# Performance work log

Hardware: AMD Instinct MI355X
Metric: run time of the kernel (lower is better)

The kernel has to match this reference:

```python
import jax, jax.numpy as jnp
import numpy as np

N = 50000      # nodes
E = 1000000    # edges (avg degree 20)
IN, H, OUT = 3, 128, 3


def setup_inputs() -> dict:
    key = jax.random.key(0)
    ks = jax.random.split(key, 12)
    pos = jax.random.normal(ks[0], (N, IN), dtype=jnp.float32)
    edge_index = jax.random.randint(ks[1], (2, E), 0, N, dtype=jnp.int64)
    dims = [(IN, H), (H, H), (H, H), (H, H), (H, OUT)]
    inp = {"pos": pos, "edge_index": edge_index}
    for i, (di, do) in enumerate(dims):
        inp[f"W{i}"] = jax.random.normal(ks[2 + 2 * i], (di, do), dtype=jnp.float32) / np.sqrt(di).astype(np.float32)
        inp[f"b{i}"] = jnp.zeros((do,), dtype=jnp.float32)
    return inp


def _gcn_conv(x, W, b, src, dst, norm):
    # PyG GCNConv: linear transform first, then normalized scatter-add, then bias
    h = x @ W                                  # [N, do]
    msg = h[src] * norm[:, None]               # gather + edge-normalize  [E+N, do]
    out = jax.ops.segment_sum(msg, dst, num_segments=N)  # scatter-add to targets
    return out + b


def reference(pos, edge_index, W0, b0, W1, b1, W2, b2, W3, b3, W4, b4):
    src, dst = edge_index[0], edge_index[1]
    loop = jnp.arange(N, dtype=src.dtype)
    src = jnp.concatenate([src, loop])         # add self-loops
    dst = jnp.concatenate([dst, loop])
    # symmetric normalization: deg computed on target nodes incl. self-loops
    deg = jax.ops.segment_sum(jnp.ones_like(src, dtype=pos.dtype), dst, num_segments=N)
    dis = jnp.where(deg > 0, jax.lax.rsqrt(jnp.maximum(deg, 1e-12)), 0.0)
    norm = dis[src] * dis[dst]                 # [E+N]

    Ws = [W0, W1, W2, W3, W4]
    bs = [b0, b1, b2, b3, b4]
    x = pos
    for i in range(4):                         # all but last layer: conv + SiLU
        x = jax.nn.silu(_gcn_conv(x, Ws[i], bs[i], src, dst, norm))
    return _gcn_conv(x, Ws[4], bs[4], src, dst, norm)
```

## Files before the change

kernel.cpp:

```cpp
#include <hip/hip_runtime.h>
#include <cstdint>
#include <cstddef>


#define NB_SPLIT 256
#define BUCKET_SHIFT 7

static __device__ __forceinline__ float silu_f(float x) {
  return x / (1.0f + __expf(-x));
}

__global__ void k_detect(const int* __restrict__ e32, int* __restrict__ flag) {
  __shared__ int any_nonzero;
  if (threadIdx.x == 0) any_nonzero = 0;
  __syncthreads();
  int v = e32[threadIdx.x * 2 + 1];
  if (v != 0) any_nonzero = 1;
  __syncthreads();
  if (threadIdx.x == 0) *flag = (any_nonzero ? 0 : 1);
}

__global__ __launch_bounds__(256) void k_prep(
    const int* __restrict__ e32, const int* __restrict__ flag,
    int* __restrict__ epack, int* __restrict__ cnt2,
    int E, int nbucket, int chunk) {
  __shared__ int hist[512];
  const int w = blockIdx.x, t = threadIdx.x;
  for (int b = t; b < nbucket; b += 256) hist[b] = 0;
  __syncthreads();
  const int f = *flag;
  const int i0 = w * chunk;
  const int i1 = min(E, i0 + chunk);
  for (int i = i0 + t; i < i1; i += 256) {
    int s, d;
    if (f) { s = e32[2 * i]; d = e32[2 * E + 2 * i]; }
    else   { s = e32[i];     d = e32[E + i]; }
    epack[i] = s | (d << 16);
    atomicAdd(&hist[d >> BUCKET_SHIFT], 1);
  }
  __syncthreads();
  for (int b = t; b < nbucket; b += 256) cnt2[b * NB_SPLIT + w] = hist[b];
}

__global__ void k_scan1(const int* __restrict__ cnt, int* __restrict__ outp,
                        int* __restrict__ bsum, int n) {
  __shared__ int wsum[4];
  const int t = threadIdx.x;
  const int base = blockIdx.x * 1024 + t * 4;
  int v0 = 0, v1 = 0, v2 = 0, v3 = 0;
  if (base + 0 < n) v0 = cnt[base + 0];
  if (base + 1 < n) v1 = cnt[base + 1];
  if (base + 2 < n) v2 = cnt[base + 2];
  if (base + 3 < n) v3 = cnt[base + 3];
  const int s = v0 + v1 + v2 + v3;
  int sc = s;
  const int lane = t & 63;
  #pragma unroll
  for (int o = 1; o < 64; o <<= 1) {
    int u = __shfl_up(sc, o);
    if (lane >= o) sc += u;
  }
  const int wid = t >> 6;
  if (lane == 63) wsum[wid] = sc;
  __syncthreads();
  int wbase = 0;
  for (int w = 0; w < wid; ++w) wbase += wsum[w];
  const int ex = wbase + sc - s;
  if (base + 0 < n) outp[base + 0] = ex;
  if (base + 1 < n) outp[base + 1] = ex + v0;
  if (base + 2 < n) outp[base + 2] = ex + v0 + v1;
  if (base + 3 < n) outp[base + 3] = ex + v0 + v1 + v2;
  if (t == 0) bsum[blockIdx.x] = wsum[0] + wsum[1] + wsum[2] + wsum[3];
}

__global__ void k_scan2(int* __restrict__ bsum, int nblk) {
  if (threadIdx.x == 0 && blockIdx.x == 0) {
    int acc = 0;
    for (int i = 0; i < nblk; ++i) { int v = bsum[i]; bsum[i] = acc; acc += v; }
  }
}

__global__ void k_scanadd(int* __restrict__ arr, const int* __restrict__ bsum, int n) {
  int i = blockIdx.x * blockDim.x + threadIdx.x;
  if (i < n) arr[i] += bsum[i >> 10];
}

__global__ __launch_bounds__(256) void k_split(
    const int* __restrict__ epack, const int* __restrict__ off2,
    int* __restrict__ tmp, int E, int nbucket, int chunk) {
  __shared__ int cur[512];
  const int w = blockIdx.x, t = threadIdx.x;
  for (int b = t; b < nbucket; b += 256) cur[b] = off2[b * NB_SPLIT + w];
  __syncthreads();
  const int i0 = w * chunk;
  const int i1 = min(E, i0 + chunk);
  for (int i = i0 + t; i < i1; i += 256) {
    int p = epack[i];
    int b = (int)(((unsigned)p) >> (16 + BUCKET_SHIFT));
    int pos = atomicAdd(&cur[b], 1);
    tmp[pos] = p;
  }
}

__global__ __launch_bounds__(256) void k_csr(
    const int* __restrict__ tmp, const int* __restrict__ off2,
    int* __restrict__ rowp, float* __restrict__ dis,
    unsigned short* __restrict__ col,
    int E, int nbucket, int N) {
  __shared__ int lcnt[128];
  __shared__ int lcur[128];
  __shared__ int wtot;
  const int b = blockIdx.x, t = threadIdx.x;
  const int nb0 = b << BUCKET_SHIFT;
  const int nn = min(1 << BUCKET_SHIFT, N - nb0);
  if (t < 128) lcnt[t] = 0;
  __syncthreads();
  const int s0 = off2[b * NB_SPLIT];
  const int s1 = (b + 1 < nbucket) ? off2[(b + 1) * NB_SPLIT] : E;
  for (int i = s0 + t; i < s1; i += 256) {
    atomicAdd(&lcnt[((unsigned)tmp[i] >> 16) & 127u], 1);
  }
  __syncthreads();
  int v = 0, sc = 0;
  if (t < 128) {
    v = lcnt[t];
    sc = v;
    #pragma unroll
    for (int o = 1; o < 64; o <<= 1) {
      int u = __shfl_up(sc, o);
      if ((t & 63) >= o) sc += u;
    }
    if (t == 63) wtot = sc;
  }
  __syncthreads();
  if (t < 128) {
    int ex = s0 + ((t >= 64) ? wtot : 0) + sc - v;
    lcur[t] = ex;
    if (t < nn) {
      rowp[nb0 + t] = ex;
      dis[nb0 + t] = rsqrtf((float)(v + 1));
    }
  }
  if (t == 0) rowp[nb0 + nn] = s1;
  __syncthreads();
  for (int i = s0 + t; i < s1; i += 256) {
    unsigned p = (unsigned)tmp[i];
    int j = (int)((p >> 16) & ((1u << BUCKET_SHIFT) - 1));
    int pos = atomicAdd(&lcur[j], 1);
    col[pos] = (unsigned short)(p & 0xffffu);
  }
}

template <int PRESCALE>
__global__ void k_agg3(const float* __restrict__ in3, float* __restrict__ out3,
                       const int* __restrict__ rowp,
                       const unsigned short* __restrict__ col,
                       const float* __restrict__ dis, const float* __restrict__ bias,
                       int n) {
  int i = blockIdx.x * blockDim.x + threadIdx.x;
  if (i >= n) return;
  const float di = dis[i];
  float a0, a1, a2;
  if (PRESCALE) {
    a0 = in3[i * 3 + 0] * di; a1 = in3[i * 3 + 1] * di; a2 = in3[i * 3 + 2] * di;
  } else {
    a0 = in3[i * 3 + 0]; a1 = in3[i * 3 + 1]; a2 = in3[i * 3 + 2];
  }
  const int e0 = rowp[i], e1 = rowp[i + 1];
  for (int e = e0; e < e1; ++e) {
    int s = col[e];
    if (PRESCALE) {
      float ds_ = dis[s];
      a0 += in3[s * 3 + 0] * ds_;
      a1 += in3[s * 3 + 1] * ds_;
      a2 += in3[s * 3 + 2] * ds_;
    } else {
      a0 += in3[s * 3 + 0];
      a1 += in3[s * 3 + 1];
      a2 += in3[s * 3 + 2];
    }
  }
  a0 *= di; a1 *= di; a2 *= di;
  if (!PRESCALE && bias) { a0 += bias[0]; a1 += bias[1]; a2 += bias[2]; }
  out3[i * 3 + 0] = a0;
  out3[i * 3 + 1] = a1;
  out3[i * 3 + 2] = a2;
}

__global__ void k_mm0(const float* __restrict__ y3, const float* __restrict__ W0,
                      const float* __restrict__ b0, const float* __restrict__ dis,
                      float* __restrict__ out, int n, int slStride) {
  int gid = blockIdx.x * blockDim.x + threadIdx.x;
  int node = gid >> 5;
  int c = (gid & 31) << 2;
  if (node >= n) return;
  float v0 = y3[node * 3 + 0], v1 = y3[node * 3 + 1], v2 = y3[node * 3 + 2];
  float4 a  = *reinterpret_cast<const float4*>(b0 + c);
  float4 w0 = *reinterpret_cast<const float4*>(W0 + 0 * 128 + c);
  float4 w1 = *reinterpret_cast<const float4*>(W0 + 1 * 128 + c);
  float4 w2 = *reinterpret_cast<const float4*>(W0 + 2 * 128 + c);
  a.x += v0 * w0.x + v1 * w1.x + v2 * w2.x;
  a.y += v0 * w0.y + v1 * w1.y + v2 * w2.y;
  a.z += v0 * w0.z + v1 * w1.z + v2 * w2.z;
  a.w += v0 * w0.w + v1 * w1.w + v2 * w2.w;
  const float d = dis[node];
  a.x = silu_f(a.x) * d; a.y = silu_f(a.y) * d;
  a.z = silu_f(a.z) * d; a.w = silu_f(a.w) * d;
  *reinterpret_cast<float4*>(out + (size_t)(c >> 4) * slStride +
                             (size_t)node * 16 + (c & 15)) = a;
}

__global__ __launch_bounds__(256) void k_agg_slice(
    const float* __restrict__ xs, float* __restrict__ y,
    const int* __restrict__ rowp, const unsigned short* __restrict__ col,
    const float* __restrict__ dis, int n, int slStride) {
  const int s = blockIdx.x & 7;
  const int nb = blockIdx.x >> 3;
  const int t = threadIdx.x;
  const int lane = t & 63;
  const int nsub = lane >> 3;
  const int ch = (lane >> 2) & 1;
  const int c4 = (lane & 3) << 2;
  const int node = nb * 32 + (t >> 6) * 8 + nsub;
  const bool valid = node < n;
  int e0 = 0, e1 = 0;
  if (valid) { e0 = rowp[node]; e1 = rowp[node + 1]; }
  const float* __restrict__ xb = xs + (size_t)s * slStride + c4;

  float4 a0 = make_float4(0.f, 0.f, 0.f, 0.f);
  float4 a1 = make_float4(0.f, 0.f, 0.f, 0.f);
  float4 a2 = make_float4(0.f, 0.f, 0.f, 0.f);
  float4 a3 = make_float4(0.f, 0.f, 0.f, 0.f);
  int e = e0 + ch;
  for (; e + 6 < e1; e += 8) {
    int s0 = col[e], s1 = col[e + 2], s2 = col[e + 4], s3 = col[e + 6];
    float4 v0 = *reinterpret_cast<const float4*>(xb + (size_t)s0 * 16);
    float4 v1 = *reinterpret_cast<const float4*>(xb + (size_t)s1 * 16);
    float4 v2 = *reinterpret_cast<const float4*>(xb + (size_t)s2 * 16);
    float4 v3 = *reinterpret_cast<const float4*>(xb + (size_t)s3 * 16);
    a0.x += v0.x; a0.y += v0.y; a0.z += v0.z; a0.w += v0.w;
    a1.x += v1.x; a1.y += v1.y; a1.z += v1.z; a1.w += v1.w;
    a2.x += v2.x; a2.y += v2.y; a2.z += v2.z; a2.w += v2.w;
    a3.x += v3.x; a3.y += v3.y; a3.z += v3.z; a3.w += v3.w;
  }
  for (; e < e1; e += 2) {
    int s0 = col[e];
    float4 v0 = *reinterpret_cast<const float4*>(xb + (size_t)s0 * 16);
    a0.x += v0.x; a0.y += v0.y; a0.z += v0.z; a0.w += v0.w;
  }
  a0.x += a1.x + a2.x + a3.x;
  a0.y += a1.y + a2.y + a3.y;
  a0.z += a1.z + a2.z + a3.z;
  a0.w += a1.w + a2.w + a3.w;
  a0.x += __shfl_xor(a0.x, 4);
  a0.y += __shfl_xor(a0.y, 4);
  a0.z += __shfl_xor(a0.z, 4);
  a0.w += __shfl_xor(a0.w, 4);
  if (valid && ch == 0) {
    float4 self = *reinterpret_cast<const float4*>(xb + (size_t)node * 16);
    const float d = dis[node];
    float4 r;
    r.x = (a0.x + self.x) * d;
    r.y = (a0.y + self.y) * d;
    r.z = (a0.z + self.z) * d;
    r.w = (a0.w + self.w) * d;
    *reinterpret_cast<float4*>(y + (size_t)s * slStride + (size_t)node * 16 + c4) = r;
  }
}

template <int PROJ>
__global__ __launch_bounds__(512) void k_mm_w(
    const float* __restrict__ x, const float* __restrict__ W,
    const float* __restrict__ bias, const float* __restrict__ dis,
    float* __restrict__ out, const float* __restrict__ W4, int n, int slStride) {
  __shared__ float ws[128][128];
  const int t = threadIdx.x;
  #pragma unroll
  for (int it = 0; it < 8; ++it) {
    int i = t + it * 512;
    *reinterpret_cast<float4*>(&ws[i >> 5][(i & 31) << 2]) =
        *reinterpret_cast<const float4*>(W + (size_t)i * 4);
  }
  __syncthreads();

  const int tc = (t & 31) << 2;
  const int tr = (t >> 5) << 2;
  const int row0 = blockIdx.x * 64;

  int rb[4];
  #pragma unroll
  for (int r = 0; r < 4; ++r) {
    rb[r] = min(row0 + tr + r, n - 1) * 16;
  }

  float4 acc[4];
  #pragma unroll
  for (int r = 0; r < 4; ++r) acc[r] = make_float4(0.f, 0.f, 0.f, 0.f);

  #pragma unroll 2
  for (int kk = 0; kk < 128; kk += 4) {
    const float* __restrict__ xk = x + (size_t)(kk >> 4) * slStride + (kk & 15);
    float4 w0 = *reinterpret_cast<const float4*>(&ws[kk + 0][tc]);
    float4 w1 = *reinterpret_cast<const float4*>(&ws[kk + 1][tc]);
    float4 w2 = *reinterpret_cast<const float4*>(&ws[kk + 2][tc]);
    float4 w3 = *reinterpret_cast<const float4*>(&ws[kk + 3][tc]);
    #pragma unroll
    for (int r = 0; r < 4; ++r) {
      float4 xr = *reinterpret_cast<const float4*>(xk + rb[r]);
      acc[r].x += xr.x * w0.x + xr.y * w1.x + xr.z * w2.x + xr.w * w3.x;
      acc[r].y += xr.x * w0.y + xr.y * w1.y + xr.z * w2.y + xr.w * w3.y;
      acc[r].z += xr.x * w0.z + xr.y * w1.z + xr.z * w2.z + xr.w * w3.z;
      acc[r].w += xr.x * w0.w + xr.y * w1.w + xr.z * w2.w + xr.w * w3.w;
    }
  }

  float4 bb = *reinterpret_cast<const float4*>(bias + tc);
  if (PROJ) {
    float w4r[4][3];
    #pragma unroll
    for (int c = 0; c < 4; ++c) {
      w4r[c][0] = W4[(tc + c) * 3 + 0];
      w4r[c][1] = W4[(tc + c) * 3 + 1];
      w4r[c][2] = W4[(tc + c) * 3 + 2];
    }
    #pragma unroll
    for (int r = 0; r < 4; ++r) {
      int row = row0 + tr + r;
      float d = (row < n) ? dis[row] : 0.0f;
      float4 a = acc[r];
      a.x = silu_f(a.x + bb.x) * d;
      a.y = silu_f(a.y + bb.y) * d;
      a.z = silu_f(a.z + bb.z) * d;
      a.w = silu_f(a.w + bb.w) * d;
      float p0 = a.x * w4r[0][0] + a.y * w4r[1][0] + a.z * w4r[2][0] + a.w * w4r[3][0];
      float p1 = a.x * w4r[0][1] + a.y * w4r[1][1] + a.z * w4r[2][1] + a.w * w4r[3][1];
      float p2 = a.x * w4r[0][2] + a.y * w4r[1][2] + a.z * w4r[2][2] + a.w * w4r[3][2];
      #pragma unroll
      for (int m = 16; m >= 1; m >>= 1) {
        p0 += __shfl_xor(p0, m);
        p1 += __shfl_xor(p1, m);
        p2 += __shfl_xor(p2, m);
      }
      if ((t & 31) == 0 && row < n) {
        out[row * 3 + 0] = p0;
        out[row * 3 + 1] = p1;
        out[row * 3 + 2] = p2;
      }
    }
  } else {
    #pragma unroll
    for (int r = 0; r < 4; ++r) {
      int row = row0 + tr + r;
      if (row < n) {
        float4 a = acc[r];
        float d = dis[row];
        a.x = silu_f(a.x + bb.x) * d;
        a.y = silu_f(a.y + bb.y) * d;
        a.z = silu_f(a.z + bb.z) * d;
        a.w = silu_f(a.w + bb.w) * d;
        *reinterpret_cast<float4*>(out + (size_t)(tc >> 4) * slStride +
                                   (size_t)row * 16 + (tc & 15)) = a;
      }
    }
  }
}

extern "C" void kernel_launch(void* const* d_in, const int* in_sizes, int n_in,
                              void* d_out, int out_size, void* d_ws, size_t ws_size,
                              hipStream_t stream) {
  const float* pos = (const float*)d_in[0];
  const int* e32 = (const int*)d_in[1];
  const float* W[5] = {(const float*)d_in[2], (const float*)d_in[4], (const float*)d_in[6],
                       (const float*)d_in[8], (const float*)d_in[10]};
  const float* B[5] = {(const float*)d_in[3], (const float*)d_in[5], (const float*)d_in[7],
                       (const float*)d_in[9], (const float*)d_in[11]};
  float* out = (float*)d_out;

  const int N = in_sizes[0] / 3;
  const int E = in_sizes[1] / 2;
  const int NBUCKET = (N + (1 << BUCKET_SHIFT) - 1) >> BUCKET_SHIFT;
  const int M = NBUCKET * NB_SPLIT;
  const int chunk = (E + NB_SPLIT - 1) / NB_SPLIT;
  const int slStride = N * 16;

  char* base = (char*)d_ws;
  size_t off = 0;
  auto alloc = [&](size_t bytes) -> void* {
    void* p = base + off;
    off += (bytes + 255) & ~(size_t)255;
    return p;
  };
  float* dis   = (float*)alloc((size_t)N * 4);
  int* rowp    = (int*)alloc((size_t)(N + 1) * 4);
  int* bsum2   = (int*)alloc(128 * 4);
  int* flag    = (int*)alloc(256);
  int* cnt2    = (int*)alloc((size_t)M * 4);
  int* off2    = (int*)alloc((size_t)M * 4);
  unsigned short* col = (unsigned short*)alloc((size_t)E * 2);
  float* y3    = (float*)alloc((size_t)N * 3 * 4);
  float* bufA  = (float*)alloc((size_t)N * 128 * 4);
  float* bufB  = (float*)alloc((size_t)N * 128 * 4);
  int* epack = (int*)bufA;
  int* tmp   = (int*)bufB;

  const int nblk2 = (M + 1023) / 1024;

  k_detect<<<1, 256, 0, stream>>>(e32, flag);
  k_prep<<<NB_SPLIT, 256, 0, stream>>>(e32, flag, epack, cnt2, E, NBUCKET, chunk);
  k_scan1<<<nblk2, 256, 0, stream>>>(cnt2, off2, bsum2, M);
  k_scan2<<<1, 64, 0, stream>>>(bsum2, nblk2);
  k_scanadd<<<(M + 255) / 256, 256, 0, stream>>>(off2, bsum2, M);
  k_split<<<NB_SPLIT, 256, 0, stream>>>(epack, off2, tmp, E, NBUCKET, chunk);
  k_csr<<<NBUCKET, 256, 0, stream>>>(tmp, off2, rowp, dis, col, E, NBUCKET, N);

  k_agg3<1><<<(N + 255) / 256, 256, 0, stream>>>(pos, y3, rowp, col, dis, nullptr, N);
  k_mm0<<<(N * 32 + 255) / 256, 256, 0, stream>>>(y3, W[0], B[0], dis, bufA, N, slStride);

  const int agg_grid = ((N + 31) / 32) * 8;
  const int mm_grid = (N + 63) / 64;
  for (int l = 1; l <= 2; ++l) {
    k_agg_slice<<<agg_grid, 256, 0, stream>>>(bufA, bufB, rowp, col, dis, N, slStride);
    k_mm_w<0><<<mm_grid, 512, 0, stream>>>(bufB, W[l], B[l], dis, bufA, nullptr, N, slStride);
  }

  k_agg_slice<<<agg_grid, 256, 0, stream>>>(bufA, bufB, rowp, col, dis, N, slStride);
  k_mm_w<1><<<mm_grid, 512, 0, stream>>>(bufB, W[3], B[3], dis, y3, W[4], N, slStride);

  k_agg3<0><<<(N + 255) / 256, 256, 0, stream>>>(y3, out, rowp, col, dis, B[4], N);

  (void)n_in; (void)out_size; (void)ws_size;
}
```

Before: 354.5 us.

## Pad CSR rows to multiples of four with dummy zero node for vectorized gathers

Pads each node's adjacency list to a multiple of four entries, filling the padding with a dummy index that points at an all-zero row appended to each feature slice. The aggregation loop can then load four column indices at once as a ushort4 and drop its remainder loop, with each half-wave handling a contiguous half of the row. This needs a CSR build split into a count pass, a serial bucket scan, and a fill pass, plus a zero-fill kernel. The separate edge-format detection kernel is folded into k_prep. The cost is extra launches, a single-threaded scan, and up to three wasted gathers per row.

```diff
diff --git a/kernel.cpp b/kernel.cpp
--- a/kernel.cpp
+++ b/kernel.cpp
@@ -10,25 +10,18 @@
   return x / (1.0f + __expf(-x));
 }
 
-__global__ void k_detect(const int* __restrict__ e32, int* __restrict__ flag) {
-  __shared__ int any_nonzero;
-  if (threadIdx.x == 0) any_nonzero = 0;
-  __syncthreads();
-  int v = e32[threadIdx.x * 2 + 1];
-  if (v != 0) any_nonzero = 1;
-  __syncthreads();
-  if (threadIdx.x == 0) *flag = (any_nonzero ? 0 : 1);
-}
-
 __global__ __launch_bounds__(256) void k_prep(
-    const int* __restrict__ e32, const int* __restrict__ flag,
-    int* __restrict__ epack, int* __restrict__ cnt2,
+    const int* __restrict__ e32, int* __restrict__ epack, int* __restrict__ cnt2,
     int E, int nbucket, int chunk) {
   __shared__ int hist[512];
+  __shared__ int nz;
   const int w = blockIdx.x, t = threadIdx.x;
   for (int b = t; b < nbucket; b += 256) hist[b] = 0;
-  __syncthreads();
-  const int f = *flag;
+  if (t == 0) nz = 0;
+  __syncthreads();
+  if (e32[t * 2 + 1] != 0) nz = 1;
+  __syncthreads();
+  const int f = nz ? 0 : 1;
   const int i0 = w * chunk;
   const int i1 = min(E, i0 + chunk);
   for (int i = i0 + t; i < i1; i += 256) {
@@ -102,29 +95,55 @@
   }
 }
 
-__global__ __launch_bounds__(256) void k_csr(
+__global__ __launch_bounds__(256) void k_csrA(
     const int* __restrict__ tmp, const int* __restrict__ off2,
+    int* __restrict__ cnt_g, int* __restrict__ bpad, int E, int nbucket) {
+  __shared__ int lcnt[128];
+  __shared__ int tot;
+  const int b = blockIdx.x, t = threadIdx.x;
+  if (t < 128) lcnt[t] = 0;
+  if (t == 0) tot = 0;
+  __syncthreads();
+  const int s0 = off2[b * NB_SPLIT];
+  const int s1 = (b + 1 < nbucket) ? off2[(b + 1) * NB_SPLIT] : E;
+  for (int i = s0 + t; i < s1; i += 256) {
+    atomicAdd(&lcnt[((unsigned)tmp[i] >> 16) & 127u], 1);
+  }
+  __syncthreads();
+  if (t < 128) {
+    int v = lcnt[t];
+    cnt_g[b * 128 + t] = v;
+    atomicAdd(&tot, (v + 3) & ~3);
+  }
+  __syncthreads();
+  if (t == 0) bpad[b] = tot;
+}
+
+__global__ void k_bscan(int* __restrict__ bpad, int nbucket,
+                        int* __restrict__ rowp, int N) {
+  if (threadIdx.x == 0 && blockIdx.x == 0) {
+    int acc = 0;
+    for (int i = 0; i < nbucket; ++i) { int v = bpad[i]; bpad[i] = acc; acc += v; }
+    bpad[nbucket] = acc;
+    rowp[N] = acc;
+  }
+}
+
+__global__ __launch_bounds__(256) void k_csrB(
+    const int* __restrict__ tmp, const int* __restrict__ off2,
+    const int* __restrict__ cnt_g, const int* __restrict__ bpad,
     int* __restrict__ rowp, float* __restrict__ dis,
-    unsigned short* __restrict__ col,
-    int E, int nbucket, int N) {
-  __shared__ int lcnt[128];
+    unsigned short* __restrict__ col, int E, int nbucket, int N) {
   __shared__ int lcur[128];
   __shared__ int wtot;
   const int b = blockIdx.x, t = threadIdx.x;
   const int nb0 = b << BUCKET_SHIFT;
   const int nn = min(1 << BUCKET_SHIFT, N - nb0);
-  if (t < 128) lcnt[t] = 0;
-  __syncthreads();
-  const int s0 = off2[b * NB_SPLIT];
-  const int s1 = (b + 1 < nbucket) ? off2[(b + 1) * NB_SPLIT] : E;
-  for (int i = s0 + t; i < s1; i += 256) {
-    atomicAdd(&lcnt[((unsigned)tmp[i] >> 16) & 127u], 1);
-  }
-  __syncthreads();
-  int v = 0, sc = 0;
+  int v = 0, pv = 0, sc = 0;
   if (t < 128) {
-    v = lcnt[t];
-    sc = v;
+    v = cnt_g[b * 128 + t];
+    pv = (v + 3) & ~3;
+    sc = pv;
     #pragma unroll
     for (int o = 1; o < 64; o <<= 1) {
       int u = __shfl_up(sc, o);
@@ -134,21 +153,31 @@
   }
   __syncthreads();
   if (t < 128) {
-    int ex = s0 + ((t >= 64) ? wtot : 0) + sc - v;
+    int ex = bpad[b] + ((t >= 64) ? wtot : 0) + sc - pv;
     lcur[t] = ex;
     if (t < nn) {
       rowp[nb0 + t] = ex;
       dis[nb0 + t] = rsqrtf((float)(v + 1));
-    }
-  }
-  if (t == 0) rowp[nb0 + nn] = s1;
-  __syncthreads();
+      for (int p = ex + v; p < ex + pv; ++p) col[p] = (unsigned short)N;
+    }
+  }
+  __syncthreads();
+  const int s0 = off2[b * NB_SPLIT];
+  const int s1 = (b + 1 < nbucket) ? off2[(b + 1) * NB_SPLIT] : E;
   for (int i = s0 + t; i < s1; i += 256) {
     unsigned p = (unsigned)tmp[i];
     int j = (int)((p >> 16) & ((1u << BUCKET_SHIFT) - 1));
     int pos = atomicAdd(&lcur[j], 1);
     col[pos] = (unsigned short)(p & 0xffffu);
   }
+}
+
+__global__ void k_zfill(float* __restrict__ bufA, float* __restrict__ bufB,
+                        int N, int slStride) {
+  const int t = threadIdx.x;
+  const int bi = t >> 7, si = (t >> 4) & 7, ci = t & 15;
+  float* bp = bi ? bufB : bufA;
+  bp[(size_t)si * slStride + (size_t)N * 16 + ci] = 0.f;
 }
 
 template <int PRESCALE>
@@ -169,6 +198,7 @@
   const int e0 = rowp[i], e1 = rowp[i + 1];
   for (int e = e0; e < e1; ++e) {
     int s = col[e];
+    if (s >= n) continue;
     if (PRESCALE) {
       float ds_ = dis[s];
       a0 += in3[s * 3 + 0] * ds_;
@@ -225,28 +255,26 @@
   const bool valid = node < n;
   int e0 = 0, e1 = 0;
   if (valid) { e0 = rowp[node]; e1 = rowp[node + 1]; }
+  const int P = e1 - e0;
+  const int h = ((P >> 1) + 3) & ~3;
+  const int eb = e0 + (ch ? h : 0);
+  const int ee = ch ? e1 : (e0 + h);
   const float* __restrict__ xb = xs + (size_t)s * slStride + c4;
 
   float4 a0 = make_float4(0.f, 0.f, 0.f, 0.f);
   float4 a1 = make_float4(0.f, 0.f, 0.f, 0.f);
   float4 a2 = make_float4(0.f, 0.f, 0.f, 0.f);
   float4 a3 = make_float4(0.f, 0.f, 0.f, 0.f);
-  int e = e0 + ch;
-  for (; e + 6 < e1; e += 8) {
-    int s0 = col[e], s1 = col[e + 2], s2 = col[e + 4], s3 = col[e + 6];
-    float4 v0 = *reinterpret_cast<const float4*>(xb + (size_t)s0 * 16);
-    float4 v1 = *reinterpret_cast<const float4*>(xb + (size_t)s1 * 16);
-    float4 v2 = *reinterpret_cast<const float4*>(xb + (size_t)s2 * 16);
-    float4 v3 = *reinterpret_cast<const float4*>(xb + (size_t)s3 * 16);
+  for (int e = eb; e < ee; e += 4) {
+    ushort4 idx = *reinterpret_cast<const ushort4*>(col + e);
+    float4 v0 = *reinterpret_cast<const float4*>(xb + (size_t)idx.x * 16);
+    float4 v1 = *reinterpret_cast<const float4*>(xb + (size_t)idx.y * 16);
+    float4 v2 = *reinterpret_cast<const float4*>(xb + (size_t)idx.z * 16);
+    float4 v3 = *reinterpret_cast<const float4*>(xb + (size_t)idx.w * 16);
     a0.x += v0.x; a0.y += v0.y; a0.z += v0.z; a0.w += v0.w;
     a1.x += v1.x; a1.y += v1.y; a1.z += v1.z; a1.w += v1.w;
     a2.x += v2.x; a2.y += v2.y; a2.z += v2.z; a2.w += v2.w;
     a3.x += v3.x; a3.y += v3.y; a3.z += v3.z; a3.w += v3.w;
-  }
-  for (; e < e1; e += 2) {
-    int s0 = col[e];
-    float4 v0 = *reinterpret_cast<const float4*>(xb + (size_t)s0 * 16);
-    a0.x += v0.x; a0.y += v0.y; a0.z += v0.z; a0.w += v0.w;
   }
   a0.x += a1.x + a2.x + a3.x;
   a0.y += a1.y + a2.y + a3.y;
@@ -381,7 +409,7 @@
   const int NBUCKET = (N + (1 << BUCKET_SHIFT) - 1) >> BUCKET_SHIFT;
   const int M = NBUCKET * NB_SPLIT;
   const int chunk = (E + NB_SPLIT - 1) / NB_SPLIT;
-  const int slStride = N * 16;
+  const int slStride = (N + 1) * 16;
 
   char* base = (char*)d_ws;
   size_t off = 0;
@@ -393,25 +421,28 @@
   float* dis   = (float*)alloc((size_t)N * 4);
   int* rowp    = (int*)alloc((size_t)(N + 1) * 4);
   int* bsum2   = (int*)alloc(128 * 4);
-  int* flag    = (int*)alloc(256);
+  int* cnt_g   = (int*)alloc((size_t)NBUCKET * 128 * 4);
+  int* bpad    = (int*)alloc((size_t)(NBUCKET + 1) * 4);
   int* cnt2    = (int*)alloc((size_t)M * 4);
   int* off2    = (int*)alloc((size_t)M * 4);
-  unsigned short* col = (unsigned short*)alloc((size_t)E * 2);
+  unsigned short* col = (unsigned short*)alloc(((size_t)E + 4 * N) * 2);
   float* y3    = (float*)alloc((size_t)N * 3 * 4);
-  float* bufA  = (float*)alloc((size_t)N * 128 * 4);
-  float* bufB  = (float*)alloc((size_t)N * 128 * 4);
+  float* bufA  = (float*)alloc((size_t)(N + 1) * 128 * 4);
+  float* bufB  = (float*)alloc((size_t)(N + 1) * 128 * 4);
   int* epack = (int*)bufA;
   int* tmp   = (int*)bufB;
 
   const int nblk2 = (M + 1023) / 1024;
 
-  k_detect<<<1, 256, 0, stream>>>(e32, flag);
-  k_prep<<<NB_SPLIT, 256, 0, stream>>>(e32, flag, epack, cnt2, E, NBUCKET, chunk);
+  k_prep<<<NB_SPLIT, 256, 0, stream>>>(e32, epack, cnt2, E, NBUCKET, chunk);
   k_scan1<<<nblk2, 256, 0, stream>>>(cnt2, off2, bsum2, M);
   k_scan2<<<1, 64, 0, stream>>>(bsum2, nblk2);
   k_scanadd<<<(M + 255) / 256, 256, 0, stream>>>(off2, bsum2, M);
   k_split<<<NB_SPLIT, 256, 0, stream>>>(epack, off2, tmp, E, NBUCKET, chunk);
-  k_csr<<<NBUCKET, 256, 0, stream>>>(tmp, off2, rowp, dis, col, E, NBUCKET, N);
+  k_csrA<<<NBUCKET, 256, 0, stream>>>(tmp, off2, cnt_g, bpad, E, NBUCKET);
+  k_bscan<<<1, 64, 0, stream>>>(bpad, NBUCKET, rowp, N);
+  k_csrB<<<NBUCKET, 256, 0, stream>>>(tmp, off2, cnt_g, bpad, rowp, dis, col, E, NBUCKET, N);
+  k_zfill<<<1, 256, 0, stream>>>(bufA, bufB, N, slStride);
 
   k_agg3<1><<<(N + 255) / 256, 256, 0, stream>>>(pos, y3, rowp, col, dis, nullptr, N);
   k_mm0<<<(N * 32 + 255) / 256, 256, 0, stream>>>(y3, W[0], B[0], dis, bufA, N, slStride);
```

Measured after the change: 391.3 us. +10.4%, slower.
